# Optimization experiments

Hardware: AMD Instinct MI355X
Metric: run time of the kernel (lower is better)

The kernel has to match this reference:

```python
import jax, jax.numpy as jnp
import numpy as np

INF = jnp.float32(1e12)  # stand-in for +inf in min-plus transform
ALPHA = 2.0


def _edt_sq_last(zero_mask):
    """Squared 1D euclidean distance along the last axis to the nearest True in zero_mask.

    zero_mask: bool (..., L). Returns float32 (..., L).
    """
    L = zero_mask.shape[-1]
    pos = jnp.arange(L)
    base = jnp.where(zero_mask, jnp.float32(0.0), INF)  # (..., L)

    def at(y):
        # min over y' of base[..., y'] + (y' - y)^2
        return jnp.min(base + (pos - y).astype(jnp.float32) ** 2, axis=-1)

    d = jax.lax.map(at, pos)  # (L, ...)
    return jnp.moveaxis(d, 0, -1)


def _edt_to(zero_mask):
    """Exact 2D euclidean distance to the nearest True pixel of zero_mask (..., H, W).

    Equivalent to scipy distance_transform_edt(~zero_mask): separable min-plus
    (parabola envelope) transform, pass over W then over H.
    """
    H = zero_mask.shape[-2]
    d1 = _edt_sq_last(zero_mask)  # squared dist along W: (..., H, W)
    rows = jnp.arange(H)

    def at(x):
        off = ((rows - x).astype(jnp.float32) ** 2)[:, None]  # (H, 1)
        return jnp.min(d1 + off, axis=-2)  # (..., W)

    D = jax.lax.map(at, rows)  # (H, ..., W)
    return jnp.sqrt(jnp.moveaxis(D, 0, -2))


def _distance_field(img):
    """Replicates HausdorffDTLoss.distance_field per (batch, channel) image.

    img: (B, C, H, W) float. fg = (img == 1). field = edt(fg) + edt(~fg),
    zero where the image has no foreground at all.
    """
    fg = img == jnp.float32(1.0)  # (B, C, H, W) bool
    has_fg = jnp.any(fg, axis=(-2, -1), keepdims=True)
    # scipy edt(mask) = distance to nearest zero of mask:
    fg_dist = _edt_to(~fg)  # edt(fg_mask)
    bg_dist = _edt_to(fg)   # edt(bg_mask)
    return jnp.where(has_fg, fg_dist + bg_dist, jnp.float32(0.0))


def setup_inputs() -> dict:
    key = jax.random.key(0)
    k1, k2 = jax.random.split(key)
    B, C, H, W = 4, 2, 384, 384
    pred = jax.random.uniform(k1, (B, C, H, W), dtype=jnp.float32)
    target = jax.random.randint(k2, (B, C, H, W), 0, 2).astype(jnp.float32)
    return {"pred": pred, "target": target}


def reference(pred, target):
    # distance fields are computed under no_grad in the original -> stop_gradient
    pred_dt = jax.lax.stop_gradient(_distance_field(pred))
    target_dt = jax.lax.stop_gradient(_distance_field(target))
    pred_error = (pred - target) ** 2
    distance = pred_dt ** ALPHA + target_dt ** ALPHA
    # per-channel means averaged over channels == global mean (equal counts)
    return jnp.mean(pred_error * distance)
```

## Files before the change

### kernel.cpp

```cpp
#include <hip/hip_runtime.h>
#include <stdint.h>

#define IMG_W 384
#define IMG_H 384
#define IMG_PIX (IMG_W * IMG_H)
#define N_IMG 16
#define SENT 0x7fff
#define BIGI (1 << 28)
#define GRID 1024
#define TPB 256
#define N_ROWS (N_IMG * IMG_H)
#define WAVES (GRID * 4)
#define PXB (N_IMG * IMG_PIX / GRID)
#define RD_MAGIC 0x5A5AC3D0u
#define PD_MAGIC 0x3C3C96E1u

static __device__ __forceinline__ uint32_t ld_a(const uint32_t* p) {
    return __hip_atomic_load(p, __ATOMIC_RELAXED, __HIP_MEMORY_SCOPE_AGENT);
}
static __device__ __forceinline__ void st_a(uint32_t* p, uint32_t v) {
    __hip_atomic_store(p, v, __ATOMIC_RELAXED, __HIP_MEMORY_SCOPE_AGENT);
}

__device__ __forceinline__ int nearest_bit_dist(const unsigned long long m[6],
                                                int wp, int b) {
    const int BIG = 1 << 20;
    int best = BIG;
    unsigned long long t = m[wp] >> b;
    if (t) best = __builtin_ctzll(t);
#pragma unroll
    for (int w = 0; w < 6; ++w) {
        if (w > wp && m[w]) {
            int cand = ((w - wp) << 6) - b + __builtin_ctzll(m[w]);
            best = min(best, cand);
        }
    }
    unsigned long long u = m[wp] << (63 - b);
    if (u) best = min(best, (int)__builtin_clzll(u));
#pragma unroll
    for (int w = 0; w < 6; ++w) {
        if (w < wp && m[w]) {
            int cand = ((wp - w - 1) << 6) + b + 1 + __builtin_clzll(m[w]);
            best = min(best, cand);
        }
    }
    return best;
}

__device__ __forceinline__ uint32_t process_row(int row, int lane,
                                                const float* __restrict__ pred,
                                                const float* __restrict__ target,
                                                uint32_t* __restrict__ d1) {
    int img = row / IMG_H;
    int x   = row - img * IMG_H;
    const float* rp = ((img < 8) ? (pred + img * IMG_PIX)
                                 : (target + (img - 8) * IMG_PIX)) + x * IMG_W;

    unsigned long long mf[6];
    bool any_fg = false;
#pragma unroll
    for (int j = 0; j < 6; ++j) {
        float v = rp[lane + 64 * j];
        mf[j] = __ballot(v == 1.0f);
        any_fg = any_fg || (mf[j] != 0ull);
    }

    uint32_t* dst = d1 + row * IMG_W;
    if (!any_fg) {
#pragma unroll
        for (int j = 0; j < 6; ++j) st_a(&dst[lane + 64 * j], (uint32_t)SENT);
        return 0u;
    }
#pragma unroll
    for (int j = 0; j < 6; ++j) {
        bool me_fg = (mf[j] >> lane) & 1ull;
        unsigned long long sm[6];
#pragma unroll
        for (int w = 0; w < 6; ++w) sm[w] = me_fg ? ~mf[w] : mf[w];
        int dv = nearest_bit_dist(sm, j, lane);
        if (dv > SENT) dv = SENT;
        st_a(&dst[lane + 64 * j], me_fg ? ((uint32_t)dv << 16) : (uint32_t)dv);
    }
    return 1u;
}

__global__ __launch_bounds__(TPB, 4) void k_fused(const float* __restrict__ pred,
                                                  const float* __restrict__ target,
                                                  uint32_t* __restrict__ d1,
                                                  uint32_t* __restrict__ rowdone,
                                                  uint32_t* __restrict__ partials,
                                                  uint32_t* __restrict__ pdone,
                                                  float* __restrict__ out) {
    int wave = threadIdx.x >> 6;
    int lane = threadIdx.x & 63;

    int g = blockIdx.x * 4 + wave;
    uint32_t fgA = process_row(g, lane, pred, target, d1);
    uint32_t fgB = 0u;
    int rowB = g + WAVES;
    if (rowB < N_ROWS) fgB = process_row(rowB, lane, pred, target, d1);
    asm volatile("s_waitcnt vmcnt(0)" ::: "memory");
    if (lane == 0) {
        st_a(&rowdone[g], RD_MAGIC | fgA);
        if (rowB < N_ROWS) st_a(&rowdone[rowB], RD_MAGIC | fgB);
    }

    int img   = blockIdx.x >> 6;
    int chunk = blockIdx.x & 63;
    __shared__ int s_flag;
    if (wave == 0) {
        const uint32_t* rd = rowdone + img * IMG_H;
        uint32_t fgacc = 0;
        for (;;) {
            uint32_t ok = 1; fgacc = 0;
#pragma unroll
            for (int j = 0; j < 6; ++j) {
                uint32_t v = ld_a(&rd[lane + 64 * j]);
                ok &= ((v & ~1u) == RD_MAGIC) ? 1u : 0u;
                fgacc |= (v & 1u);
            }
            if (__all(ok != 0)) break;
            __builtin_amdgcn_s_sleep(2);
        }
        int f = __any(fgacc != 0) ? 1 : 0;
        if (lane == 0) s_flag = f;
    }
    __syncthreads();
    bool flag = (s_flag != 0);

    float contrib = 0.0f;
    if (flag) {
        const uint32_t* d = d1 + img * IMG_PIX;
        const float* pp = pred   + (img & 7) * IMG_PIX;
        const float* tp = target + (img & 7) * IMG_PIX;
        int base = chunk * PXB + threadIdx.x;
#pragma unroll
        for (int gs = 0; gs < 3; ++gs) {
            uint32_t c0[3], cm1[3], cp1[3], cm2[3], cp2[3];
            float pv[3], tv[3];
            int xs[3], ys[3];
#pragma unroll
            for (int t = 0; t < 3; ++t) {
                int pid = base + (gs * 3 + t) * TPB;
                int x = pid / IMG_W, y = pid - x * IMG_W;
                xs[t] = x; ys[t] = y;
                pv[t] = pp[pid]; tv[t] = tp[pid];
                int xm1 = (x > 0) ? x - 1 : 0;
                int xp1 = (x < IMG_H - 1) ? x + 1 : IMG_H - 1;
                int xm2 = (x > 1) ? x - 2 : 0;
                int xp2 = (x < IMG_H - 2) ? x + 2 : IMG_H - 1;
                c0 [t] = ld_a(&d[pid]);
                cm1[t] = ld_a(&d[xm1 * IMG_W + y]);
                cp1[t] = ld_a(&d[xp1 * IMG_W + y]);
                cm2[t] = ld_a(&d[xm2 * IMG_W + y]);
                cp2[t] = ld_a(&d[xp2 * IMG_W + y]);
            }
#pragma unroll
            for (int t = 0; t < 3; ++t) {
                int f0 = (int)(c0[t] & 0xffffu), b0 = (int)(c0[t] >> 16);
                int bf = (f0 >= SENT) ? BIGI : f0 * f0;
                int bb = (b0 >= SENT) ? BIGI : b0 * b0;
                auto acc = [&](uint32_t cc, int kk) {
                    int f = (int)(cc & 0xffffu), b2 = (int)(cc >> 16);
                    if (f  < SENT) bf = min(bf, f * f + kk);
                    if (b2 < SENT) bb = min(bb, b2 * b2 + kk);
                };
                acc(cm1[t], 1); acc(cp1[t], 1); acc(cm2[t], 4); acc(cp2[t], 4);
                int x = xs[t], y = ys[t];
                int k = 3, kk = 9;
                while ((kk < bf || kk < bb) && k < IMG_H) {
                    int xm = x - k, xp = x + k;
                    if (xm >= 0)    acc(ld_a(&d[xm * IMG_W + y]), kk);
                    if (xp < IMG_H) acc(ld_a(&d[xp * IMG_W + y]), kk);
                    ++k;
                    kk = k * k;
                }
                float dbf = (bf >= BIGI) ? 1e12f : (float)bf;
                float dbb = (bb >= BIGI) ? 1e12f : (float)bb;
                float e = pv[t] - tv[t];
                contrib += e * e * (dbf + dbb);
            }
        }
    }

    for (int o = 32; o > 0; o >>= 1) contrib += __shfl_down(contrib, o);
    __shared__ float part[4];
    if (lane == 0) part[wave] = contrib;
    __syncthreads();
    if (threadIdx.x == 0) {
        float s = part[0] + part[1] + part[2] + part[3];
        st_a(&partials[blockIdx.x], __float_as_uint(s));
        asm volatile("s_waitcnt vmcnt(0)" ::: "memory");
        st_a(&pdone[blockIdx.x], PD_MAGIC);
    }

    if (blockIdx.x == GRID - 1) {
        for (;;) {
            uint32_t ok = 1;
#pragma unroll
            for (int t = 0; t < 4; ++t)
                ok &= (ld_a(&pdone[threadIdx.x + 256 * t]) == PD_MAGIC) ? 1u : 0u;
            if (__syncthreads_and((int)ok)) break;
            __builtin_amdgcn_s_sleep(2);
        }
        double s = 0.0;
#pragma unroll
        for (int t = 0; t < 4; ++t)
            s += (double)__uint_as_float(ld_a(&partials[threadIdx.x + 256 * t]));
        for (int o = 32; o > 0; o >>= 1) s += __shfl_down(s, o);
        __shared__ double dpart[4];
        if (lane == 0) dpart[wave] = s;
        __syncthreads();
        if (threadIdx.x == 0)
            out[0] = (float)((dpart[0] + dpart[1] + dpart[2] + dpart[3]) *
                             (1.0 / (double)(8 * IMG_PIX)));
    }
}

extern "C" void kernel_launch(void* const* d_in, const int* in_sizes, int n_in,
                              void* d_out, int out_size, void* d_ws, size_t ws_size,
                              hipStream_t stream) {
    const float* pred   = (const float*)d_in[0];
    const float* target = (const float*)d_in[1];
    char* ws = (char*)d_ws;
    uint32_t* rowdone  = (uint32_t*)ws;
    uint32_t* pdone    = (uint32_t*)(ws + 32768);
    uint32_t* partials = (uint32_t*)(ws + 40960);
    uint32_t* d1       = (uint32_t*)(ws + 65536);

    k_fused<<<GRID, TPB, 0, stream>>>(pred, target, d1, rowdone, partials,
                                      pdone, (float*)d_out);
}
```

Before: 19.08 us.

## Give each block its own rows with halo in LDS, synchronizing only on demand

Each block now computes the row-wise distance pass for its own 6 rows plus a 2-row halo and keeps them in LDS. The column pass reads neighbours from LDS and only waits on specific remote rows, via per-row flags, when its search leaves the local window. This replaces the old per-image barrier, where every block waited for all 384 rows of its image, and removes most global reloads of d1. The cost is that halo rows are computed redundantly, and occupancy may drop from the 15KB LDS buffer.

```diff
diff --git a/kernel.cpp b/kernel.cpp
--- a/kernel.cpp
+++ b/kernel.cpp
@@ -9,9 +9,10 @@
 #define BIGI (1 << 28)
 #define GRID 1024
 #define TPB 256
-#define N_ROWS (N_IMG * IMG_H)
-#define WAVES (GRID * 4)
-#define PXB (N_IMG * IMG_PIX / GRID)
+#define ROWS_PER_BLK 6
+#define HALO 2
+#define LROWS (ROWS_PER_BLK + 2 * HALO)
+#define PXB (ROWS_PER_BLK * IMG_W)
 #define RD_MAGIC 0x5A5AC3D0u
 #define PD_MAGIC 0x3C3C96E1u
 
@@ -45,43 +46,6 @@
         }
     }
     return best;
-}
-
-__device__ __forceinline__ uint32_t process_row(int row, int lane,
-                                                const float* __restrict__ pred,
-                                                const float* __restrict__ target,
-                                                uint32_t* __restrict__ d1) {
-    int img = row / IMG_H;
-    int x   = row - img * IMG_H;
-    const float* rp = ((img < 8) ? (pred + img * IMG_PIX)
-                                 : (target + (img - 8) * IMG_PIX)) + x * IMG_W;
-
-    unsigned long long mf[6];
-    bool any_fg = false;
-#pragma unroll
-    for (int j = 0; j < 6; ++j) {
-        float v = rp[lane + 64 * j];
-        mf[j] = __ballot(v == 1.0f);
-        any_fg = any_fg || (mf[j] != 0ull);
-    }
-
-    uint32_t* dst = d1 + row * IMG_W;
-    if (!any_fg) {
-#pragma unroll
-        for (int j = 0; j < 6; ++j) st_a(&dst[lane + 64 * j], (uint32_t)SENT);
-        return 0u;
-    }
-#pragma unroll
-    for (int j = 0; j < 6; ++j) {
-        bool me_fg = (mf[j] >> lane) & 1ull;
-        unsigned long long sm[6];
-#pragma unroll
-        for (int w = 0; w < 6; ++w) sm[w] = me_fg ? ~mf[w] : mf[w];
-        int dv = nearest_bit_dist(sm, j, lane);
-        if (dv > SENT) dv = SENT;
-        st_a(&dst[lane + 64 * j], me_fg ? ((uint32_t)dv << 16) : (uint32_t)dv);
-    }
-    return 1u;
 }
 
 __global__ __launch_bounds__(TPB, 4) void k_fused(const float* __restrict__ pred,
@@ -91,104 +55,170 @@
                                                   uint32_t* __restrict__ partials,
                                                   uint32_t* __restrict__ pdone,
                                                   float* __restrict__ out) {
+    __shared__ uint32_t lds[LROWS][IMG_W];
+    __shared__ int s_ownfg;
+    __shared__ int s_flag;
+    __shared__ float s_part[4];
+
     int wave = threadIdx.x >> 6;
     int lane = threadIdx.x & 63;
-
-    int g = blockIdx.x * 4 + wave;
-    uint32_t fgA = process_row(g, lane, pred, target, d1);
-    uint32_t fgB = 0u;
-    int rowB = g + WAVES;
-    if (rowB < N_ROWS) fgB = process_row(rowB, lane, pred, target, d1);
+    int img  = blockIdx.x >> 6;
+    int chunk = blockIdx.x & 63;
+    int x0 = chunk * ROWS_PER_BLK;
+
+    if (threadIdx.x == 0) s_ownfg = 0;
+    __syncthreads();
+
+    const float* src = (img < 8) ? (pred + img * IMG_PIX)
+                                 : (target + (img - 8) * IMG_PIX);
+
+    int own_gx[2], own_fg[2], n_own = 0;
+    int wave_fg = 0;
+    for (int rl = wave; rl < LROWS; rl += 4) {
+        int gx = x0 - HALO + rl;
+        if (gx < 0 || gx >= IMG_H) {
+#pragma unroll
+            for (int j = 0; j < 6; ++j)
+                lds[rl][lane + 64 * j] = (uint32_t)SENT | ((uint32_t)SENT << 16);
+            continue;
+        }
+        const float* rp = src + gx * IMG_W;
+        unsigned long long mf[6];
+        bool any = false;
+#pragma unroll
+        for (int j = 0; j < 6; ++j) {
+            float v = rp[lane + 64 * j];
+            mf[j] = __ballot(v == 1.0f);
+            any = any || (mf[j] != 0ull);
+        }
+        bool own = (rl >= HALO) && (rl < HALO + ROWS_PER_BLK);
+        uint32_t* gdst = d1 + (size_t)(img * IMG_H + gx) * IMG_W;
+        if (!any) {
+#pragma unroll
+            for (int j = 0; j < 6; ++j) {
+                lds[rl][lane + 64 * j] = (uint32_t)SENT;
+                if (own) st_a(&gdst[lane + 64 * j], (uint32_t)SENT);
+            }
+        } else {
+            wave_fg = 1;
+#pragma unroll
+            for (int j = 0; j < 6; ++j) {
+                bool me_fg = (mf[j] >> lane) & 1ull;
+                unsigned long long sm[6];
+#pragma unroll
+                for (int w = 0; w < 6; ++w) sm[w] = me_fg ? ~mf[w] : mf[w];
+                int dv = nearest_bit_dist(sm, j, lane);
+                if (dv > SENT) dv = SENT;
+                uint32_t val = me_fg ? ((uint32_t)dv << 16) : (uint32_t)dv;
+                lds[rl][lane + 64 * j] = val;
+                if (own) st_a(&gdst[lane + 64 * j], val);
+            }
+        }
+        if (own) { own_gx[n_own] = gx; own_fg[n_own] = any ? 1 : 0; ++n_own; }
+    }
     asm volatile("s_waitcnt vmcnt(0)" ::: "memory");
     if (lane == 0) {
-        st_a(&rowdone[g], RD_MAGIC | fgA);
-        if (rowB < N_ROWS) st_a(&rowdone[rowB], RD_MAGIC | fgB);
-    }
-
-    int img   = blockIdx.x >> 6;
-    int chunk = blockIdx.x & 63;
-    __shared__ int s_flag;
-    if (wave == 0) {
-        const uint32_t* rd = rowdone + img * IMG_H;
-        uint32_t fgacc = 0;
-        for (;;) {
-            uint32_t ok = 1; fgacc = 0;
-#pragma unroll
-            for (int j = 0; j < 6; ++j) {
-                uint32_t v = ld_a(&rd[lane + 64 * j]);
-                ok &= ((v & ~1u) == RD_MAGIC) ? 1u : 0u;
-                fgacc |= (v & 1u);
-            }
-            if (__all(ok != 0)) break;
-            __builtin_amdgcn_s_sleep(2);
-        }
-        int f = __any(fgacc != 0) ? 1 : 0;
-        if (lane == 0) s_flag = f;
+        for (int i = 0; i < n_own; ++i)
+            st_a(&rowdone[img * IMG_H + own_gx[i]], RD_MAGIC | (uint32_t)own_fg[i]);
+        if (wave_fg) atomicOr(&s_ownfg, 1);
     }
     __syncthreads();
-    bool flag = (s_flag != 0);
+
+    bool flag;
+    if (s_ownfg) {
+        flag = true;
+    } else {
+        if (wave == 0) {
+            const uint32_t* rd = rowdone + img * IMG_H;
+            uint32_t fgacc = 0;
+            for (;;) {
+                uint32_t ok = 1; fgacc = 0;
+#pragma unroll
+                for (int j = 0; j < 6; ++j) {
+                    uint32_t v = ld_a(&rd[lane + 64 * j]);
+                    ok &= ((v & ~1u) == RD_MAGIC) ? 1u : 0u;
+                    fgacc |= (v & 1u);
+                }
+                if (__all(ok != 0)) break;
+                __builtin_amdgcn_s_sleep(2);
+            }
+            if (lane == 0) s_flag = __any(fgacc != 0) ? 1 : 0;
+        }
+        __syncthreads();
+        flag = (s_flag != 0);
+    }
 
     float contrib = 0.0f;
     if (flag) {
-        const uint32_t* d = d1 + img * IMG_PIX;
         const float* pp = pred   + (img & 7) * IMG_PIX;
         const float* tp = target + (img & 7) * IMG_PIX;
-        int base = chunk * PXB + threadIdx.x;
-#pragma unroll
-        for (int gs = 0; gs < 3; ++gs) {
-            uint32_t c0[3], cm1[3], cp1[3], cm2[3], cp2[3];
-            float pv[3], tv[3];
-            int xs[3], ys[3];
-#pragma unroll
-            for (int t = 0; t < 3; ++t) {
-                int pid = base + (gs * 3 + t) * TPB;
-                int x = pid / IMG_W, y = pid - x * IMG_W;
-                xs[t] = x; ys[t] = y;
-                pv[t] = pp[pid]; tv[t] = tp[pid];
-                int xm1 = (x > 0) ? x - 1 : 0;
-                int xp1 = (x < IMG_H - 1) ? x + 1 : IMG_H - 1;
-                int xm2 = (x > 1) ? x - 2 : 0;
-                int xp2 = (x < IMG_H - 2) ? x + 2 : IMG_H - 1;
-                c0 [t] = ld_a(&d[pid]);
-                cm1[t] = ld_a(&d[xm1 * IMG_W + y]);
-                cp1[t] = ld_a(&d[xp1 * IMG_W + y]);
-                cm2[t] = ld_a(&d[xm2 * IMG_W + y]);
-                cp2[t] = ld_a(&d[xp2 * IMG_W + y]);
-            }
-#pragma unroll
-            for (int t = 0; t < 3; ++t) {
-                int f0 = (int)(c0[t] & 0xffffu), b0 = (int)(c0[t] >> 16);
-                int bf = (f0 >= SENT) ? BIGI : f0 * f0;
-                int bb = (b0 >= SENT) ? BIGI : b0 * b0;
-                auto acc = [&](uint32_t cc, int kk) {
-                    int f = (int)(cc & 0xffffu), b2 = (int)(cc >> 16);
-                    if (f  < SENT) bf = min(bf, f * f + kk);
-                    if (b2 < SENT) bb = min(bb, b2 * b2 + kk);
-                };
-                acc(cm1[t], 1); acc(cp1[t], 1); acc(cm2[t], 4); acc(cp2[t], 4);
-                int x = xs[t], y = ys[t];
-                int k = 3, kk = 9;
-                while ((kk < bf || kk < bb) && k < IMG_H) {
-                    int xm = x - k, xp = x + k;
-                    if (xm >= 0)    acc(ld_a(&d[xm * IMG_W + y]), kk);
-                    if (xp < IMG_H) acc(ld_a(&d[xp * IMG_W + y]), kk);
-                    ++k;
-                    kk = k * k;
+        float pv[9], tv[9];
+#pragma unroll
+        for (int t = 0; t < 9; ++t) {
+            int pid = chunk * PXB + t * TPB + threadIdx.x;
+            pv[t] = pp[pid];
+            tv[t] = tp[pid];
+        }
+#pragma unroll
+        for (int t = 0; t < 9; ++t) {
+            int pid = chunk * PXB + t * TPB + threadIdx.x;
+            int x = pid / IMG_W;
+            int y = pid - x * IMG_W;
+            int rl = x - x0 + HALO;
+            uint32_t c0 = lds[rl][y];
+            int f0 = (int)(c0 & 0xffffu), b0 = (int)(c0 >> 16);
+            int bf = (f0 >= SENT) ? BIGI : f0 * f0;
+            int bb = (b0 >= SENT) ? BIGI : b0 * b0;
+            auto acc = [&](uint32_t cc, int kk) {
+                int f = (int)(cc & 0xffffu), b2 = (int)(cc >> 16);
+                if (f  < SENT) bf = min(bf, f * f + kk);
+                if (b2 < SENT) bb = min(bb, b2 * b2 + kk);
+            };
+            acc(lds[rl - 1][y], 1); acc(lds[rl + 1][y], 1);
+            acc(lds[rl - 2][y], 4); acc(lds[rl + 2][y], 4);
+
+            int k = 3, kk = 9;
+            while ((kk < bf || kk < bb) && k < IMG_H) {
+                int xm = x - k, xp = x + k;
+                if (xm >= 0) {
+                    int xr = xm - (x0 - HALO);
+                    uint32_t cc;
+                    if (xr >= 0 && xr < LROWS) cc = lds[xr][y];
+                    else {
+                        const uint32_t* rd = &rowdone[img * IMG_H + xm];
+                        while ((ld_a(rd) & ~1u) != RD_MAGIC)
+                            __builtin_amdgcn_s_sleep(1);
+                        cc = ld_a(&d1[(size_t)(img * IMG_H + xm) * IMG_W + y]);
+                    }
+                    acc(cc, kk);
                 }
-                float dbf = (bf >= BIGI) ? 1e12f : (float)bf;
-                float dbb = (bb >= BIGI) ? 1e12f : (float)bb;
-                float e = pv[t] - tv[t];
-                contrib += e * e * (dbf + dbb);
-            }
+                if (xp < IMG_H) {
+                    int xr = xp - (x0 - HALO);
+                    uint32_t cc;
+                    if (xr >= 0 && xr < LROWS) cc = lds[xr][y];
+                    else {
+                        const uint32_t* rd = &rowdone[img * IMG_H + xp];
+                        while ((ld_a(rd) & ~1u) != RD_MAGIC)
+                            __builtin_amdgcn_s_sleep(1);
+                        cc = ld_a(&d1[(size_t)(img * IMG_H + xp) * IMG_W + y]);
+                    }
+                    acc(cc, kk);
+                }
+                ++k;
+                kk = k * k;
+            }
+            float dbf = (bf >= BIGI) ? 1e12f : (float)bf;
+            float dbb = (bb >= BIGI) ? 1e12f : (float)bb;
+            float e = pv[t] - tv[t];
+            contrib += e * e * (dbf + dbb);
         }
     }
 
     for (int o = 32; o > 0; o >>= 1) contrib += __shfl_down(contrib, o);
-    __shared__ float part[4];
-    if (lane == 0) part[wave] = contrib;
+    if (lane == 0) s_part[wave] = contrib;
     __syncthreads();
     if (threadIdx.x == 0) {
-        float s = part[0] + part[1] + part[2] + part[3];
+        float s = s_part[0] + s_part[1] + s_part[2] + s_part[3];
         st_a(&partials[blockIdx.x], __float_as_uint(s));
         asm volatile("s_waitcnt vmcnt(0)" ::: "memory");
         st_a(&pdone[blockIdx.x], PD_MAGIC);
```

New measurement: 18.30 us. -4.0%, faster.
